# Performance work log

Measured on AMD Instinct MI355X. Metric: run time of the kernel, lower is better.

## Reference

```python
import jax, jax.numpy as jnp
import numpy as np

N = 64
K_CHEB = 5
EPS = 1e-5

# db4 decomposition filters (scaling_filter.mat Lo_D / Hi_D, length 8)
_LO = np.array([-0.010597401784997278, 0.032883011666982945, 0.030841381835986965,
                -0.18703481171888114, -0.02798376941698385, 0.6308807679295904,
                0.7148465705525415, 0.23037781330885523], dtype=np.float32)
_HI = np.array([-0.23037781330885523, 0.7148465705525415, -0.6308807679295904,
                -0.02798376941698385, 0.18703481171888114, 0.030841381835986965,
                0.032883011666982945, -0.010597401784997278], dtype=np.float32)
# torch stores np.flip(filters) and Conv2d does cross-correlation -> use flipped taps here too
_KERN = np.stack([_LO[::-1], _HI[::-1]])[:, None, None, :].copy()  # [2,1,1,8]


def _wavelet_step(x):
    # x: [B, C, 1, W]; circular pad 3 each side, depthwise len-8 conv, stride 2
    p = 3  # filter_length // 2 - 1
    xp = jnp.concatenate([x[..., -p:], x, x[..., :p]], axis=-1)
    b, c, h, wp = xp.shape
    out = jax.lax.conv_general_dilated(
        xp.reshape(b * c, 1, h, wp), jnp.asarray(_KERN), (1, 2), 'VALID',
        dimension_numbers=('NCHW', 'OIHW', 'NCHW'))
    out = out.reshape(b, c, 2, h, -1)
    return out[:, :, 0], out[:, :, 1]  # (approx, detail)


def _cbam(x, fc1, fc2, sa_w):
    # x: [B, 657, 1, 64]; channel attention then spatial attention
    def mlp(v):  # v: [B, C, 1, 1]
        h = jax.nn.relu(jnp.einsum('oc,bchw->bohw', fc1, v))
        return jnp.einsum('oc,bchw->bohw', fc2, h)
    avg = x.mean(axis=(2, 3), keepdims=True)
    mx = x.max(axis=(2, 3), keepdims=True)
    x = x * jax.nn.sigmoid(mlp(avg) + mlp(mx))
    s = jnp.concatenate([x.mean(axis=1, keepdims=True), x.max(axis=1, keepdims=True)], axis=1)
    sa = jax.nn.sigmoid(jax.lax.conv_general_dilated(
        s, sa_w, (1, 1), ((3, 3), (3, 3)), dimension_numbers=('NCHW', 'OIHW', 'NCHW')))
    return x * sa


def _global_edge_weight(w_tril, mask):
    xs, ys = np.tril_indices(N)
    E = jnp.zeros((N, N), w_tril.dtype).at[xs, ys].set(w_tril)
    E = E + E.T - jnp.diag(jnp.diag(E))
    return (E * mask).reshape(-1)


def _norm_adj(edges, w):
    # PyG NewSGConv.norm: add remaining self-loops (fill=1), deg from |w|, sym normalize
    row, col = edges[0], edges[1]
    has_self = jnp.zeros((N,), w.dtype).at[row].add(jnp.where(row == col, 1.0, 0.0)) > 0
    w_self = jnp.where(has_self, 0.0, 1.0).astype(w.dtype)
    deg = jnp.zeros((N,), w.dtype).at[row].add(jnp.abs(w)) + w_self
    dsafe = jnp.where(deg > 0, deg, 1.0)
    dinv = jnp.where(deg > 0, jax.lax.rsqrt(dsafe), 0.0)
    norm = dinv[row] * w * dinv[col]
    A = jnp.zeros((N, N), w.dtype).at[col, row].add(norm)  # out[i] = sum_j A[i,j] x[j]
    return A + jnp.diag(dinv * w_self * dinv)


def _gcn_block(x, A, W, b, g, be):
    # x: [B, N, C_in]; K-hop SGConv propagation, linear, train-mode batchnorm over (B, N)
    for _ in range(K_CHEB):
        x = jnp.einsum('ij,bjc->bic', A, x)
    x = x @ W.T + b
    mean = x.mean(axis=(0, 1))
    var = x.var(axis=(0, 1))
    return (x - mean) * jax.lax.rsqrt(var + EPS) * g + be


def _classify(x, W1, b1, g, be, W2, b2):
    out = x.reshape(x.shape[0], -1) @ W1.T + b1
    out = (out - out.mean(0)) * jax.lax.rsqrt(out.var(0) + EPS) * g + be
    return jax.nn.log_softmax(out @ W2.T + b2, axis=1)


def _forward(x, local_graph_weight, global_mask, ca_fc1, ca_fc2, sa_conv, edge_weight_tril,
             ld_W, ld_b, ld_g, ld_be, ld1_W, ld1_b, ld1_g, ld1_be,
             d_W, d_b, d_g, d_be, d1_W, d1_b, d1_g, d1_be,
             cls_W1, cls_b1, cls_g, cls_be, cls_W2, cls_b2, edges):
    xc = jnp.transpose(x, (0, 3, 2, 1))        # [B, 657, 1, 64]
    xc = _cbam(xc, ca_fc1, ca_fc2, sa_conv)
    xh = jnp.transpose(xc, (0, 3, 2, 1))       # [B, 64, 1, 657]
    # fi = floor(log2(200)) = 7 -> 4 decomposition levels: 657->328->164->82->41
    out1, _gamma = _wavelet_step(xh)
    out2, _beta = _wavelet_step(out1)
    out3, _alpha = _wavelet_step(out2)
    delta, _theta = _wavelet_step(out3)        # [B, 64, 1, 41]
    delta = delta[:, :, 0, :]                  # squeeze -> [B, 64, 41]
    gw = _global_edge_weight(edge_weight_tril, global_mask)
    A_loc = _norm_adj(edges, local_graph_weight)
    A_glb = _norm_adj(edges, gw)
    lf = _gcn_block(delta, A_loc, ld_W, ld_b, ld_g, ld_be)
    lf = _gcn_block(lf, A_loc, ld1_W, ld1_b, ld1_g, ld1_be)
    gf = _gcn_block(delta, A_glb, d_W, d_b, d_g, d_be)
    gf = _gcn_block(gf, A_glb, d1_W, d1_b, d1_g, d1_be)
    feat = jnp.concatenate([lf.mean(-1, keepdims=True), gf.mean(-1, keepdims=True)], axis=2)  # [B,64,2]
    return _classify(feat, cls_W1, cls_b1, cls_g, cls_be, cls_W2, cls_b2)


def setup_inputs() -> dict:
    key = jax.random.key(0)
    ks = iter(jax.random.split(key, 16))
    B = 512
    f32 = jnp.float32
    def rn(shape, s=0.05):
        return jax.random.normal(next(ks), shape, f32) * s
    ii = jnp.arange(N, dtype=jnp.int32)
    edges = jnp.stack([jnp.repeat(ii, N), jnp.tile(ii, N)])  # full 64x64 mesh (incl. self loops)
    return dict(
        x=jax.random.normal(next(ks), (B, N, 1, 657), f32),
        local_graph_weight=jax.random.uniform(next(ks), (N * N,), f32),
        global_mask=jnp.ones((N, N), f32),
        ca_fc1=rn((82, 657)),
        ca_fc2=rn((657, 82)),
        sa_conv=rn((1, 2, 7, 7), 0.1),
        edge_weight_tril=jax.random.uniform(next(ks), (N * (N + 1) // 2,), f32),
        ld_W=rn((16, 41)), ld_b=jnp.zeros(16, f32), ld_g=jnp.ones(16, f32), ld_be=jnp.zeros(16, f32),
        ld1_W=rn((4, 16)), ld1_b=jnp.zeros(4, f32), ld1_g=jnp.ones(4, f32), ld1_be=jnp.zeros(4, f32),
        d_W=rn((16, 41)), d_b=jnp.zeros(16, f32), d_g=jnp.ones(16, f32), d_be=jnp.zeros(16, f32),
        d1_W=rn((4, 16)), d1_b=jnp.zeros(4, f32), d1_g=jnp.ones(4, f32), d1_be=jnp.zeros(4, f32),
        cls_W1=rn((32, 128)), cls_b1=jnp.zeros(32, f32), cls_g=jnp.ones(32, f32), cls_be=jnp.zeros(32, f32),
        cls_W2=rn((2, 32)), cls_b2=jnp.zeros(2, f32),
        edges=edges,
    )


def reference(x, local_graph_weight, global_mask, ca_fc1, ca_fc2, sa_conv, edge_weight_tril,
              ld_W, ld_b, ld_g, ld_be, ld1_W, ld1_b, ld1_g, ld1_be,
              d_W, d_b, d_g, d_be, d1_W, d1_b, d1_g, d1_be,
              cls_W1, cls_b1, cls_g, cls_be, cls_W2, cls_b2, edges):
    return _forward(x, local_graph_weight, global_mask, ca_fc1, ca_fc2, sa_conv, edge_weight_tril,
                    ld_W, ld_b, ld_g, ld_be, ld1_W, ld1_b, ld1_g, ld1_be,
                    d_W, d_b, d_g, d_be, d1_W, d1_b, d1_g, d1_be,
                    cls_W1, cls_b1, cls_g, cls_be, cls_W2, cls_b2, edges)
```

## Files before the change

### kernel.cpp

```cpp
#include <hip/hip_runtime.h>
#include <math.h>

#define NB 512
#define NN 64
#define TL 657
#define LV1 328
#define LV2 164
#define LV3 82
#define LV4 41
#define HID 82
#define ST 66

#define WS_M      0
#define WS_ACC    32768
#define WS_SMEAN  36864
#define WS_SMAX   167936
#define WS_FC2T   299008
#define WS_CSUM   682496
#define WS_CMAX   2028032
#define WS_CATT   3373568
#define WS_Y1     682496
#define WS_DELTA  4876800
#define WS_Y2     4876800
#define WS_OUT1   5925376

#define ACC_Y1 0
#define ACC_Y2 64
#define ACC_O1 80

__device__ __forceinline__ float sigmoidf_(float v){ return 1.0f/(1.0f+expf(-v)); }

__device__ __forceinline__ void wav_level(float* __restrict__ dst, const float* __restrict__ src,
                                          int outL, int inL, int lane){
  const float DLO[8] = {0.23037781330885523f, 0.7148465705525415f, 0.6308807679295904f,
                        -0.02798376941698385f, -0.18703481171888114f, 0.030841381835986965f,
                        0.032883011666982945f, -0.010597401784997278f};
  for (int k=lane; k<outL; k+=64){
    int i0 = 2*k - 3;
    float a = 0.f;
    #pragma unroll
    for (int j=0;j<8;j++){
      int idx = i0 + j;
      idx = (idx < 0) ? idx + inL : ((idx >= inL) ? idx - inL : idx);
      a += src[idx]*DLO[j];
    }
    dst[k] = a;
  }
}

__device__ __forceinline__ void mm8(float* __restrict__ D, int dstride,
                                    const float* __restrict__ A, const float* __restrict__ Bm){
  int tid = threadIdx.x;
  int wv = tid >> 6, lane = tid & 63;
  int i0 = wv*8;
  float acc8[8];
  #pragma unroll
  for (int i=0;i<8;i++) acc8[i]=0.f;
  #pragma unroll
  for (int kc=0; kc<4; kc++){
    float bb[16];
    #pragma unroll
    for (int j=0;j<16;j++) bb[j] = Bm[(kc*16+j)*ST + lane];
    #pragma unroll
    for (int i=0;i<8;i++){
      const float2* ar = (const float2*)&A[(i0+i)*ST + kc*16];
      float s0=0.f, s1=0.f;
      #pragma unroll
      for (int j2=0;j2<8;j2++){
        float2 v = ar[j2];
        s0 += v.x*bb[2*j2]; s1 += v.y*bb[2*j2+1];
      }
      acc8[i] += s0+s1;
    }
  }
  #pragma unroll
  for (int i=0;i<8;i++) D[(i0+i)*dstride + lane] = acc8[i];
}

__global__ __launch_bounds__(512) void k_front(
    const float* __restrict__ x,
    const float* __restrict__ lgw, const float* __restrict__ gmask,
    const float* __restrict__ tril, const int* __restrict__ edges,
    const float* __restrict__ fc2,
    float* __restrict__ csum, float* __restrict__ cmax,
    float* __restrict__ Mout, float* __restrict__ fc2T,
    double* __restrict__ acc)
{
  __shared__ float smem[3*NN*ST];
  __shared__ float deg[64], hs[64], dinv[64], wself[64];
  int tid = threadIdx.x;
  int bid = blockIdx.x;

  if (bid < NB){
    int b = bid;
    int wv = tid>>6, lane = tid&63;
    float s[11], m[11];
    #pragma unroll
    for (int i=0;i<11;i++){ s[i]=0.f; m[i]=-INFINITY; }
    const float* xb = x + (size_t)b*NN*TL;
    for (int r=0;r<8;r++){
      const float* row = xb + (size_t)(wv*8 + r)*TL;
      #pragma unroll
      for (int i=0;i<11;i++){
        int t = lane + 64*i;
        if (t < TL){
          float v = row[t];
          s[i] += v; m[i] = fmaxf(m[i], v);
        }
      }
    }
    float* buf = smem;
    for (int step=4; step>=1; step>>=1){
      if (wv >= step && wv < 2*step){
        float* bs = buf + (wv-step)*2*664;
        #pragma unroll
        for (int i=0;i<11;i++){
          int t = lane + 64*i;
          if (t<TL){ bs[t] = s[i]; bs[664+t] = m[i]; }
        }
      }
      __syncthreads();
      if (wv < step){
        float* bs = buf + wv*2*664;
        #pragma unroll
        for (int i=0;i<11;i++){
          int t = lane + 64*i;
          if (t<TL){ s[i] += bs[t]; m[i] = fmaxf(m[i], bs[664+t]); }
        }
      }
      __syncthreads();
    }
    if (wv==0){
      #pragma unroll
      for (int i=0;i<11;i++){
        int t = lane + 64*i;
        if (t<TL){
          csum[(size_t)b*TL + t] = s[i];
          cmax[(size_t)b*TL + t] = m[i];
        }
      }
    }
    return;
  }

  int gi = bid - NB;
  if (gi >= 2){
    int t8 = gi - 2;
    int r0 = t8*83;
    int rn = (t8==7) ? (TL - 7*83) : 83;
    for (int i=tid; i<rn*HID; i+=512){
      int r = i / HID, u = i - r*HID;
      smem[u*85 + r] = fc2[(size_t)r0*HID + i];
    }
    __syncthreads();
    for (int j=tid; j<HID*83; j+=512){
      int u = j / 83, c = j - u*83;
      if (c < rn) fc2T[u*TL + r0 + c] = smem[u*85 + c];
    }
    return;
  }

  float* Wbuf = smem;
  float* Amat = smem + NN*ST;
  float* P1   = smem + 2*NN*ST;
  int g = gi;
  if (g==0 && tid<512) acc[tid]=0.0;
  for (int e=tid;e<4096;e+=512){
    float w;
    if (g==0) w = lgw[e];
    else {
      int i=e>>6, j=e&63;
      int aa = (i>j)? i:j, bb = (i>j)? j:i;
      w = tril[aa*(aa+1)/2 + bb] * gmask[e];
    }
    Wbuf[e] = w;
  }
  for (int i=tid;i<NN*ST;i+=512) Amat[i] = 0.f;
  if (tid<64){ deg[tid]=0.f; hs[tid]=0.f; }
  __syncthreads();
  {
    int e0 = tid*8;
    int runr = edges[e0];
    float runv = 0.f;
    #pragma unroll 4
    for (int i=0;i<8;i++){
      int e = e0+i;
      int r = edges[e];
      int c = edges[4096+e];
      float w = Wbuf[e];
      if (r != runr){ atomicAdd(&deg[runr], runv); runr = r; runv = 0.f; }
      runv += fabsf(w);
      if (r == c) hs[r] = 1.f;
    }
    atomicAdd(&deg[runr], runv);
  }
  __syncthreads();
  if (tid<64){
    float w_ = (hs[tid] > 0.f) ? 0.f : 1.f;
    float d = deg[tid] + w_;
    dinv[tid] = (d > 0.f) ? rsqrtf(d) : 0.f;
    wself[tid] = w_;
  }
  __syncthreads();
  for (int e=tid;e<4096;e+=512){
    int r = edges[e], c = edges[4096+e];
    float nm = dinv[r]*Wbuf[e]*dinv[c];
    atomicAdd(&Amat[c*ST+r], nm);
  }
  __syncthreads();
  if (tid<64) Amat[tid*ST+tid] += dinv[tid]*wself[tid]*dinv[tid];
  __syncthreads();
  mm8(P1,   ST, Amat, Amat); __syncthreads();
  mm8(Wbuf, ST, P1,   P1);   __syncthreads();
  mm8(&Mout[g*4096], 64, Wbuf, Amat);
}

__global__ __launch_bounds__(512) void k_mlp(
    const float* __restrict__ csum, const float* __restrict__ cmax,
    const float* __restrict__ fc1, const float* __restrict__ fc2T,
    float* __restrict__ catt)
{
  __shared__ float cs[TL], cm[TL];
  __shared__ float h[HID];
  int tid = threadIdx.x, b = blockIdx.x;
  for (int i=tid;i<TL;i+=512){
    cs[i] = csum[(size_t)b*TL + i];
    cm[i] = cmax[(size_t)b*TL + i];
  }
  __syncthreads();
  int wv = tid>>6, lane = tid&63;
  for (int o=wv; o<HID; o+=8){
    const float* fr = fc1 + (size_t)o*TL;
    float a = 0.f, bm = 0.f;
    #pragma unroll
    for (int i=0;i<11;i++){
      int c = lane + 64*i;
      if (c < TL){
        float f = fr[c];
        a += f*cs[c]; bm += f*cm[c];
      }
    }
    #pragma unroll
    for (int off=32;off;off>>=1){
      a  += __shfl_xor(a,off);
      bm += __shfl_xor(bm,off);
    }
    if (lane==0)
      h[o] = fmaxf(a*(1.0f/64.0f),0.f) + fmaxf(bm,0.f);
  }
  __syncthreads();
  for (int c=tid;c<TL;c+=512){
    float a=0.f;
    #pragma unroll 4
    for (int u=0;u<HID;u++) a += fc2T[(size_t)u*TL + c]*h[u];
    catt[(size_t)b*TL + c] = sigmoidf_(a);
  }
}

__global__ __launch_bounds__(256) void k_wav(
    const float* __restrict__ x, const float* __restrict__ catt_g,
    float* __restrict__ delta, float* __restrict__ smean, float* __restrict__ smax)
{
  __shared__ float catt[TL];
  __shared__ float yb[4][TL];
  __shared__ float o1b[4][LV1];
  __shared__ float o2b[4][LV2];
  __shared__ float o3b[4][LV3];
  int tid = threadIdx.x, b = blockIdx.x;
  for (int i=tid;i<TL;i+=256) catt[i] = catt_g[(size_t)b*TL + i];
  __syncthreads();
  int wv = tid>>6, lane = tid&63;
  int n = blockIdx.y*4 + wv;
  float* y  = yb[wv];
  float* p1 = o1b[wv];
  float* p2 = o2b[wv];
  float* p3 = o3b[wv];
  const float DLO[8] = {0.23037781330885523f, 0.7148465705525415f, 0.6308807679295904f,
                        -0.02798376941698385f, -0.18703481171888114f, 0.030841381835986965f,
                        0.032883011666982945f, -0.010597401784997278f};
  const float* row = x + ((size_t)b*NN + n)*TL;
  float ls = 0.f, lm = -INFINITY;
  #pragma unroll
  for (int i=0;i<11;i++){
    int t = lane + 64*i;
    if (t < TL){
      float v = row[t]*catt[t];
      y[t] = v; ls += v; lm = fmaxf(lm,v);
    }
  }
  #pragma unroll
  for (int off=32;off;off>>=1){
    ls += __shfl_xor(ls,off);
    lm = fmaxf(lm, __shfl_xor(lm,off));
  }
  if (lane==0){ smean[b*NN+n] = ls*(1.0f/657.0f); smax[b*NN+n] = lm; }
  wav_level(p1, y,  LV1, TL,  lane);
  wav_level(p2, p1, LV2, LV1, lane);
  wav_level(p3, p2, LV3, LV2, lane);
  if (lane < LV4){
    int i0 = 2*lane - 3;
    float a = 0.f;
    #pragma unroll
    for (int j=0;j<8;j++){
      int idx = i0 + j;
      idx = (idx < 0) ? idx + LV3 : ((idx >= LV3) ? idx - LV3 : idx);
      a += p3[idx]*DLO[j];
    }
    delta[((size_t)b*NN + n)*LV4 + lane] = a;
  }
}

__global__ __launch_bounds__(256) void k_gcn1(
  const float* __restrict__ delta, const float* __restrict__ Mmat,
  const float* __restrict__ smean, const float* __restrict__ smax,
  const float* __restrict__ saw,
  const float* __restrict__ ldW, const float* __restrict__ ldb,
  const float* __restrict__ dW, const float* __restrict__ db2,
  float* __restrict__ Y1, double* __restrict__ acc)
{
  __shared__ float Dl[NN*LV4];
  __shared__ float Tt[NN*16];
  __shared__ float Mm[4096];
  __shared__ float Wl[16*LV4];
  __shared__ float satt[NN];
  __shared__ double red[256];
  int tid=threadIdx.x, b=blockIdx.x;
  if (tid < NN){
    float a = 0.f;
    #pragma unroll
    for (int kw=0;kw<7;kw++){
      int w = tid + kw - 3;
      if (0<=w && w<NN) a += smean[b*NN+w]*saw[21+kw] + smax[b*NN+w]*saw[70+kw];
    }
    satt[tid] = sigmoidf_(a);
  }
  __syncthreads();
  const float* ds = delta + (size_t)b*NN*LV4;
  for (int i=tid;i<NN*LV4;i+=256) Dl[i] = ds[i]*satt[i/LV4];
  for (int g=0; g<2; g++){
    const float* Ws = g ? dW : ldW;
    const float* bs = g ? db2 : ldb;
    for (int i=tid;i<16*LV4;i+=256) Wl[i]=Ws[i];
    for (int i=tid;i<4096;i+=256) Mm[i]=Mmat[g*4096+i];
    __syncthreads();
    for (int e=tid;e<NN*16;e+=256){
      int n=e>>4, o=e&15;
      const float* dr=&Dl[n*LV4];
      const float* wr=&Wl[o*LV4];
      float a=0.f;
      #pragma unroll 8
      for (int c=0;c<LV4;c++) a += dr[c]*wr[c];
      Tt[e]=a;
    }
    __syncthreads();
    float bias = bs[tid&15];
    float ps=0.f, pq=0.f;
    for (int m=0;m<4;m++){
      int e=tid+256*m;
      int n=e>>4, o=e&15;
      float a=bias;
      #pragma unroll 8
      for (int k=0;k<64;k++) a += Mm[n*64+k]*Tt[k*16+o];
      Y1[((size_t)b*NN+n)*32 + g*16 + o] = a;
      ps += a; pq += a*a;
    }
    red[tid]=(double)ps;
    __syncthreads();
    if (tid<16){ double t=0; for (int r=tid;r<256;r+=16) t+=red[r]; atomicAdd(&acc[ACC_Y1+g*32+tid], t); }
    __syncthreads();
    red[tid]=(double)pq;
    __syncthreads();
    if (tid<16){ double t=0; for (int r=tid;r<256;r+=16) t+=red[r]; atomicAdd(&acc[ACC_Y1+g*32+16+tid], t); }
    __syncthreads();
  }
}

__global__ __launch_bounds__(256) void k_gcn2(
  const float* __restrict__ Y1, const float* __restrict__ Mmat,
  const float* __restrict__ ldg, const float* __restrict__ ldbe,
  const float* __restrict__ dg, const float* __restrict__ dbe,
  const float* __restrict__ ld1W, const float* __restrict__ ld1b,
  const float* __restrict__ d1W, const float* __restrict__ d1b,
  float* __restrict__ Y2, double* __restrict__ acc)
{
  __shared__ float Yl[NN*32];
  __shared__ float T2[NN*8];
  __shared__ float Mm[2*4096];
  __shared__ float scl[32], sht[32];
  __shared__ double red[256];
  int tid=threadIdx.x, b=blockIdx.x;
  const float* ys = Y1 + (size_t)b*NN*32;
  for (int i=tid;i<NN*32;i+=256) Yl[i]=ys[i];
  for (int i=tid;i<8192;i+=256) Mm[i]=Mmat[i];
  if (tid<32){
    int g=tid>>4, o=tid&15;
    double s=acc[ACC_Y1+g*32+o], q=acc[ACC_Y1+g*32+16+o];
    double mean=s/32768.0;
    double var=q/32768.0 - mean*mean;
    float gam = g? dg[o] : ldg[o];
    float bet = g? dbe[o] : ldbe[o];
    float sc = gam * rsqrtf((float)var + 1e-5f);
    scl[tid]=sc; sht[tid]=bet - (float)mean*sc;
  }
  __syncthreads();
  for (int i=tid;i<NN*32;i+=256){ int c=i&31; Yl[i]=Yl[i]*scl[c]+sht[c]; }
  __syncthreads();
  for (int e=tid;e<NN*8;e+=256){
    int n=e>>3, c=e&7, g=c>>2, p=c&3;
    const float* w = (g? d1W : ld1W) + p*16;
    const float* yr = &Yl[n*32 + g*16];
    float a=0.f;
    #pragma unroll
    for (int o=0;o<16;o++) a += yr[o]*w[o];
    T2[e]=a;
  }
  __syncthreads();
  float ps=0.f,pq=0.f;
  for (int m=0;m<2;m++){
    int e=tid+256*m;
    int n=e>>3, c=e&7, g=c>>2;
    float a = g? d1b[c&3] : ld1b[c&3];
    const float* mr=&Mm[g*4096+n*64];
    #pragma unroll 8
    for (int k=0;k<64;k++) a += mr[k]*T2[k*8+c];
    Y2[((size_t)b*NN+n)*8 + c] = a;
    ps+=a; pq+=a*a;
  }
  red[tid]=(double)ps; __syncthreads();
  if (tid<8){ double t=0; for (int r=tid;r<256;r+=8) t+=red[r]; atomicAdd(&acc[ACC_Y2 + (tid>>2)*8 + (tid&3)], t); }
  __syncthreads();
  red[tid]=(double)pq; __syncthreads();
  if (tid<8){ double t=0; for (int r=tid;r<256;r+=8) t+=red[r]; atomicAdd(&acc[ACC_Y2 + (tid>>2)*8 + 4 + (tid&3)], t); }
}

__global__ __launch_bounds__(64) void k_featcls(
  const float* __restrict__ Y2,
  const float* __restrict__ ld1g, const float* __restrict__ ld1be,
  const float* __restrict__ d1g, const float* __restrict__ d1be,
  const float* __restrict__ W1, const float* __restrict__ b1,
  float* __restrict__ out1, double* __restrict__ acc)
{
  __shared__ float f[128];
  __shared__ float scl[8], sht[8];
  int tid=threadIdx.x, b=blockIdx.x;
  if (tid<8){
    int g=tid>>2, p=tid&3;
    double s=acc[ACC_Y2+g*8+p], q=acc[ACC_Y2+g*8+4+p];
    double mean=s/32768.0;
    double var=q/32768.0-mean*mean;
    float gam = g? d1g[p]:ld1g[p];
    float bet = g? d1be[p]:ld1be[p];
    float sc = gam*rsqrtf((float)var+1e-5f);
    scl[tid]=sc; sht[tid]=bet-(float)mean*sc;
  }
  __syncthreads();
  {
    const float* yr = Y2 + ((size_t)b*NN+tid)*8;
    float lf=0.f, gf=0.f;
    #pragma unroll
    for (int p=0;p<4;p++){
      lf += yr[p]*scl[p]+sht[p];
      gf += yr[4+p]*scl[4+p]+sht[4+p];
    }
    f[2*tid]   = lf*0.25f;
    f[2*tid+1] = gf*0.25f;
  }
  __syncthreads();
  if (tid<32){
    const float* w = W1 + tid*128;
    float a = b1[tid];
    #pragma unroll 4
    for (int m=0;m<128;m++) a += w[m]*f[m];
    out1[b*32+tid]=a;
    atomicAdd(&acc[ACC_O1+tid], (double)a);
    atomicAdd(&acc[ACC_O1+32+tid], (double)(a*a));
  }
}

__global__ __launch_bounds__(64) void k_cls2(
  const float* __restrict__ out1,
  const float* __restrict__ cg, const float* __restrict__ cbe,
  const float* __restrict__ W2, const float* __restrict__ b2,
  const double* __restrict__ acc, float* __restrict__ out)
{
  __shared__ float v[32];
  __shared__ float z[2];
  int tid=threadIdx.x, b=blockIdx.x;
  if (tid<32){
    double s=acc[ACC_O1+tid], q=acc[ACC_O1+32+tid];
    double mean=s/512.0;
    double var=q/512.0-mean*mean;
    float sc=cg[tid]*rsqrtf((float)var+1e-5f);
    float sh=cbe[tid]-(float)mean*sc;
    v[tid]=out1[b*32+tid]*sc+sh;
  }
  __syncthreads();
  if (tid<2){
    const float* w=W2+tid*32;
    float a=b2[tid];
    #pragma unroll
    for (int j=0;j<32;j++) a += w[j]*v[j];
    z[tid]=a;
  }
  __syncthreads();
  if (tid<2){
    float m=fmaxf(z[0],z[1]);
    float l=m+logf(expf(z[0]-m)+expf(z[1]-m));
    out[b*2+tid]=z[tid]-l;
  }
}

extern "C" void kernel_launch(void* const* d_in, const int* in_sizes, int n_in,
                              void* d_out, int out_size, void* d_ws, size_t ws_size,
                              hipStream_t stream) {
  (void)in_sizes; (void)n_in; (void)out_size; (void)ws_size;
  const float* x     = (const float*)d_in[0];
  const float* lgw   = (const float*)d_in[1];
  const float* gmask = (const float*)d_in[2];
  const float* fc1   = (const float*)d_in[3];
  const float* fc2   = (const float*)d_in[4];
  const float* saw   = (const float*)d_in[5];
  const float* tril  = (const float*)d_in[6];
  const float* ldW   = (const float*)d_in[7];
  const float* ldb   = (const float*)d_in[8];
  const float* ldg   = (const float*)d_in[9];
  const float* ldbe  = (const float*)d_in[10];
  const float* ld1W  = (const float*)d_in[11];
  const float* ld1b  = (const float*)d_in[12];
  const float* ld1g  = (const float*)d_in[13];
  const float* ld1be = (const float*)d_in[14];
  const float* dW    = (const float*)d_in[15];
  const float* db2   = (const float*)d_in[16];
  const float* dg    = (const float*)d_in[17];
  const float* dbe   = (const float*)d_in[18];
  const float* d1W   = (const float*)d_in[19];
  const float* d1b   = (const float*)d_in[20];
  const float* d1g   = (const float*)d_in[21];
  const float* d1be  = (const float*)d_in[22];
  const float* cW1   = (const float*)d_in[23];
  const float* cb1   = (const float*)d_in[24];
  const float* cgam  = (const float*)d_in[25];
  const float* cbet  = (const float*)d_in[26];
  const float* cW2   = (const float*)d_in[27];
  const float* cb2   = (const float*)d_in[28];
  const int*   edges = (const int*)d_in[29];

  char* ws = (char*)d_ws;
  float*  M     = (float*)(ws + WS_M);
  double* acc   = (double*)(ws + WS_ACC);
  float*  smean = (float*)(ws + WS_SMEAN);
  float*  smax  = (float*)(ws + WS_SMAX);
  float*  fc2T  = (float*)(ws + WS_FC2T);
  float*  csum  = (float*)(ws + WS_CSUM);
  float*  cmax  = (float*)(ws + WS_CMAX);
  float*  catt  = (float*)(ws + WS_CATT);
  float*  Y1    = (float*)(ws + WS_Y1);
  float*  delta = (float*)(ws + WS_DELTA);
  float*  Y2    = (float*)(ws + WS_Y2);
  float*  out1  = (float*)(ws + WS_OUT1);
  float*  out   = (float*)d_out;

  k_front<<<NB + 10, 512, 0, stream>>>(x, lgw, gmask, tril, edges, fc2,
                                       csum, cmax, M, fc2T, acc);
  k_mlp<<<NB, 512, 0, stream>>>(csum, cmax, fc1, fc2T, catt);
  k_wav<<<dim3(NB, 16), 256, 0, stream>>>(x, catt, delta, smean, smax);
  k_gcn1<<<NB, 256, 0, stream>>>(delta, M, smean, smax, saw, ldW, ldb, dW, db2, Y1, acc);
  k_gcn2<<<NB, 256, 0, stream>>>(Y1, M, ldg, ldbe, dg, dbe, ld1W, ld1b, d1W, d1b, Y2, acc);
  k_featcls<<<NB, 64, 0, stream>>>(Y2, ld1g, ld1be, d1g, d1be, cW1, cb1, out1, acc);
  k_cls2<<<NB, 64, 0, stream>>>(out1, cgam, cbet, cW2, cb2, acc, out);
}
```

Before: 184.1 us.

## Fuse channel-attention MLP into front reduction kernel with 1024-thread blocks

Merges the channel-attention MLP (fc1/fc2 plus sigmoid) into the per-batch channel reduction block, so the csum/cmax workspace round trip, the fc2 transpose blocks and one kernel launch are removed. Blocks grow to 1024 threads, with a deeper wave reduction tree, and the graph-matrix blocks now give each wave 4 rows instead of 8. fc2 is now read untransposed as float2 per output channel, which gives strided global reads across threads. Larger blocks may lower occupancy during the x-reduction phase.

```diff
diff --git a/kernel.cpp b/kernel.cpp
--- a/kernel.cpp
+++ b/kernel.cpp
@@ -15,9 +15,6 @@
 #define WS_ACC    32768
 #define WS_SMEAN  36864
 #define WS_SMAX   167936
-#define WS_FC2T   299008
-#define WS_CSUM   682496
-#define WS_CMAX   2028032
 #define WS_CATT   3373568
 #define WS_Y1     682496
 #define WS_DELTA  4876800
@@ -48,21 +45,19 @@
   }
 }
 
-__device__ __forceinline__ void mm8(float* __restrict__ D, int dstride,
-                                    const float* __restrict__ A, const float* __restrict__ Bm){
+__device__ __forceinline__ void mm16(float* __restrict__ D, int dstride,
+                                     const float* __restrict__ A, const float* __restrict__ Bm){
   int tid = threadIdx.x;
   int wv = tid >> 6, lane = tid & 63;
-  int i0 = wv*8;
-  float acc8[8];
-  #pragma unroll
-  for (int i=0;i<8;i++) acc8[i]=0.f;
+  int i0 = wv*4;
+  float a4[4] = {0.f,0.f,0.f,0.f};
   #pragma unroll
   for (int kc=0; kc<4; kc++){
     float bb[16];
     #pragma unroll
     for (int j=0;j<16;j++) bb[j] = Bm[(kc*16+j)*ST + lane];
     #pragma unroll
-    for (int i=0;i<8;i++){
+    for (int i=0;i<4;i++){
       const float2* ar = (const float2*)&A[(i0+i)*ST + kc*16];
       float s0=0.f, s1=0.f;
       #pragma unroll
@@ -70,36 +65,35 @@
         float2 v = ar[j2];
         s0 += v.x*bb[2*j2]; s1 += v.y*bb[2*j2+1];
       }
-      acc8[i] += s0+s1;
+      a4[i] += s0+s1;
     }
   }
   #pragma unroll
-  for (int i=0;i<8;i++) D[(i0+i)*dstride + lane] = acc8[i];
-}
-
-__global__ __launch_bounds__(512) void k_front(
+  for (int i=0;i<4;i++) D[(i0+i)*dstride + lane] = a4[i];
+}
+
+__global__ __launch_bounds__(1024) void k_front(
     const float* __restrict__ x,
     const float* __restrict__ lgw, const float* __restrict__ gmask,
     const float* __restrict__ tril, const int* __restrict__ edges,
-    const float* __restrict__ fc2,
-    float* __restrict__ csum, float* __restrict__ cmax,
-    float* __restrict__ Mout, float* __restrict__ fc2T,
-    double* __restrict__ acc)
+    const float* __restrict__ fc1, const float* __restrict__ fc2,
+    float* __restrict__ catt_g,
+    float* __restrict__ Mout, double* __restrict__ acc)
 {
   __shared__ float smem[3*NN*ST];
   __shared__ float deg[64], hs[64], dinv[64], wself[64];
   int tid = threadIdx.x;
   int bid = blockIdx.x;
-
-  if (bid < NB){
-    int b = bid;
-    int wv = tid>>6, lane = tid&63;
+  int wv = tid>>6, lane = tid&63;
+
+  if (bid >= 2){
+    int b = bid - 2;
     float s[11], m[11];
     #pragma unroll
     for (int i=0;i<11;i++){ s[i]=0.f; m[i]=-INFINITY; }
     const float* xb = x + (size_t)b*NN*TL;
-    for (int r=0;r<8;r++){
-      const float* row = xb + (size_t)(wv*8 + r)*TL;
+    for (int r=0;r<4;r++){
+      const float* row = xb + (size_t)(wv*4 + r)*TL;
       #pragma unroll
       for (int i=0;i<11;i++){
         int t = lane + 64*i;
@@ -109,10 +103,9 @@
         }
       }
     }
-    float* buf = smem;
-    for (int step=4; step>=1; step>>=1){
+    for (int step=8; step>=1; step>>=1){
       if (wv >= step && wv < 2*step){
-        float* bs = buf + (wv-step)*2*664;
+        float* bs = smem + (wv-step)*1328;
         #pragma unroll
         for (int i=0;i<11;i++){
           int t = lane + 64*i;
@@ -121,7 +114,7 @@
       }
       __syncthreads();
       if (wv < step){
-        float* bs = buf + wv*2*664;
+        float* bs = smem + wv*1328;
         #pragma unroll
         for (int i=0;i<11;i++){
           int t = lane + 64*i;
@@ -130,32 +123,46 @@
       }
       __syncthreads();
     }
+    float* cs = smem;
+    float* cm = smem + 664;
+    float* h  = smem + 1400;
     if (wv==0){
       #pragma unroll
       for (int i=0;i<11;i++){
         int t = lane + 64*i;
-        if (t<TL){
-          csum[(size_t)b*TL + t] = s[i];
-          cmax[(size_t)b*TL + t] = m[i];
+        if (t<TL){ cs[t] = s[i]; cm[t] = m[i]; }
+      }
+    }
+    __syncthreads();
+    for (int o=wv; o<HID; o+=16){
+      const float* fr = fc1 + (size_t)o*TL;
+      float a = 0.f, bm = 0.f;
+      #pragma unroll
+      for (int i=0;i<11;i++){
+        int c = lane + 64*i;
+        if (c < TL){
+          float f = fr[c];
+          a += f*cs[c]; bm += f*cm[c];
         }
       }
-    }
-    return;
-  }
-
-  int gi = bid - NB;
-  if (gi >= 2){
-    int t8 = gi - 2;
-    int r0 = t8*83;
-    int rn = (t8==7) ? (TL - 7*83) : 83;
-    for (int i=tid; i<rn*HID; i+=512){
-      int r = i / HID, u = i - r*HID;
-      smem[u*85 + r] = fc2[(size_t)r0*HID + i];
-    }
-    __syncthreads();
-    for (int j=tid; j<HID*83; j+=512){
-      int u = j / 83, c = j - u*83;
-      if (c < rn) fc2T[u*TL + r0 + c] = smem[u*85 + c];
+      #pragma unroll
+      for (int off=32;off;off>>=1){
+        a  += __shfl_xor(a,off);
+        bm += __shfl_xor(bm,off);
+      }
+      if (lane==0)
+        h[o] = fmaxf(a*(1.0f/64.0f),0.f) + fmaxf(bm,0.f);
+    }
+    __syncthreads();
+    if (tid < TL){
+      const float2* fr = (const float2*)(fc2 + (size_t)tid*HID);
+      float a0=0.f, a1=0.f;
+      #pragma unroll
+      for (int u2=0;u2<41;u2++){
+        float2 v = fr[u2];
+        a0 += v.x*h[2*u2]; a1 += v.y*h[2*u2+1];
+      }
+      catt_g[(size_t)b*TL + tid] = sigmoidf_(a0+a1);
     }
     return;
   }
@@ -163,9 +170,9 @@
   float* Wbuf = smem;
   float* Amat = smem + NN*ST;
   float* P1   = smem + 2*NN*ST;
-  int g = gi;
+  int g = bid;
   if (g==0 && tid<512) acc[tid]=0.0;
-  for (int e=tid;e<4096;e+=512){
+  for (int e=tid;e<4096;e+=1024){
     float w;
     if (g==0) w = lgw[e];
     else {
@@ -175,15 +182,15 @@
     }
     Wbuf[e] = w;
   }
-  for (int i=tid;i<NN*ST;i+=512) Amat[i] = 0.f;
+  for (int i=tid;i<NN*ST;i+=1024) Amat[i] = 0.f;
   if (tid<64){ deg[tid]=0.f; hs[tid]=0.f; }
   __syncthreads();
   {
-    int e0 = tid*8;
+    int e0 = tid*4;
     int runr = edges[e0];
     float runv = 0.f;
-    #pragma unroll 4
-    for (int i=0;i<8;i++){
+    #pragma unroll
+    for (int i=0;i<4;i++){
       int e = e0+i;
       int r = edges[e];
       int c = edges[4096+e];
@@ -202,7 +209,7 @@
     wself[tid] = w_;
   }
   __syncthreads();
-  for (int e=tid;e<4096;e+=512){
+  for (int e=tid;e<4096;e+=1024){
     int r = edges[e], c = edges[4096+e];
     float nm = dinv[r]*Wbuf[e]*dinv[c];
     atomicAdd(&Amat[c*ST+r], nm);
@@ -210,51 +217,9 @@
   __syncthreads();
   if (tid<64) Amat[tid*ST+tid] += dinv[tid]*wself[tid]*dinv[tid];
   __syncthreads();
-  mm8(P1,   ST, Amat, Amat); __syncthreads();
-  mm8(Wbuf, ST, P1,   P1);   __syncthreads();
-  mm8(&Mout[g*4096], 64, Wbuf, Amat);
-}
-
-__global__ __launch_bounds__(512) void k_mlp(
-    const float* __restrict__ csum, const float* __restrict__ cmax,
-    const float* __restrict__ fc1, const float* __restrict__ fc2T,
-    float* __restrict__ catt)
-{
-  __shared__ float cs[TL], cm[TL];
-  __shared__ float h[HID];
-  int tid = threadIdx.x, b = blockIdx.x;
-  for (int i=tid;i<TL;i+=512){
-    cs[i] = csum[(size_t)b*TL + i];
-    cm[i] = cmax[(size_t)b*TL + i];
-  }
-  __syncthreads();
-  int wv = tid>>6, lane = tid&63;
-  for (int o=wv; o<HID; o+=8){
-    const float* fr = fc1 + (size_t)o*TL;
-    float a = 0.f, bm = 0.f;
-    #pragma unroll
-    for (int i=0;i<11;i++){
-      int c = lane + 64*i;
-      if (c < TL){
-        float f = fr[c];
-        a += f*cs[c]; bm += f*cm[c];
-      }
-    }
-    #pragma unroll
-    for (int off=32;off;off>>=1){
-      a  += __shfl_xor(a,off);
-      bm += __shfl_xor(bm,off);
-    }
-    if (lane==0)
-      h[o] = fmaxf(a*(1.0f/64.0f),0.f) + fmaxf(bm,0.f);
-  }
-  __syncthreads();
-  for (int c=tid;c<TL;c+=512){
-    float a=0.f;
-    #pragma unroll 4
-    for (int u=0;u<HID;u++) a += fc2T[(size_t)u*TL + c]*h[u];
-    catt[(size_t)b*TL + c] = sigmoidf_(a);
-  }
+  mm16(P1,   ST, Amat, Amat); __syncthreads();
+  mm16(Wbuf, ST, P1,   P1);   __syncthreads();
+  mm16(&Mout[g*4096], 64, Wbuf, Amat);
 }
 
 __global__ __launch_bounds__(256) void k_wav(
@@ -550,9 +515,6 @@
   double* acc   = (double*)(ws + WS_ACC);
   float*  smean = (float*)(ws + WS_SMEAN);
   float*  smax  = (float*)(ws + WS_SMAX);
-  float*  fc2T  = (float*)(ws + WS_FC2T);
-  float*  csum  = (float*)(ws + WS_CSUM);
-  float*  cmax  = (float*)(ws + WS_CMAX);
   float*  catt  = (float*)(ws + WS_CATT);
   float*  Y1    = (float*)(ws + WS_Y1);
   float*  delta = (float*)(ws + WS_DELTA);
@@ -560,9 +522,8 @@
   float*  out1  = (float*)(ws + WS_OUT1);
   float*  out   = (float*)d_out;
 
-  k_front<<<NB + 10, 512, 0, stream>>>(x, lgw, gmask, tril, edges, fc2,
-                                       csum, cmax, M, fc2T, acc);
-  k_mlp<<<NB, 512, 0, stream>>>(csum, cmax, fc1, fc2T, catt);
+  k_front<<<NB + 2, 1024, 0, stream>>>(x, lgw, gmask, tril, edges, fc1, fc2,
+                                       catt, M, acc);
   k_wav<<<dim3(NB, 16), 256, 0, stream>>>(x, catt, delta, smean, smax);
   k_gcn1<<<NB, 256, 0, stream>>>(delta, M, smean, smax, saw, ldW, ldb, dW, db2, Y1, acc);
   k_gcn2<<<NB, 256, 0, stream>>>(Y1, M, ldg, ldbe, dg, dbe, ld1W, ld1b, d1W, d1b, Y2, acc);
```

Result: faster. 162.8 us (-11.6%).
